# Optimization experiments

Measured on AMD Instinct MI355X. Metric: run time of the kernel, lower is better.

Reference implementation:

```python
import jax, jax.numpy as jnp
import numpy as np

N_NODES = 100000
N_EDGES = 200000
N_GRAPHS = 4000
F_IN = 44
H = 256
E = 512
L = 4


def setup_inputs() -> dict:
    key = jax.random.key(0)
    ks = jax.random.split(key, 16)
    x = jax.random.normal(ks[0], (N_NODES, F_IN), dtype=jnp.float32)
    edge_index = jax.random.randint(ks[1], (2, N_EDGES), 0, N_NODES)
    batch = jnp.sort(jax.random.randint(ks[2], (N_NODES,), 0, N_GRAPHS))
    s = lambda fan_in: 1.0 / np.sqrt(fan_in)
    W_atom = jax.random.uniform(ks[3], (F_IN, H), jnp.float32, -s(F_IN), s(F_IN))
    b_atom = jnp.zeros((H,), jnp.float32)
    W1 = jax.random.uniform(ks[4], (L, H, 2 * H), jnp.float32, -s(H), s(H))
    b1 = jnp.zeros((L, 2 * H), jnp.float32)
    W2 = jax.random.uniform(ks[5], (L, 2 * H, H), jnp.float32, -s(2 * H), s(2 * H))
    b2 = jnp.zeros((L, H), jnp.float32)
    Wf1 = jax.random.uniform(ks[6], (H, H), jnp.float32, -s(H), s(H))
    bf1 = jnp.zeros((H,), jnp.float32)
    Wf2 = jax.random.uniform(ks[7], (H, E), jnp.float32, -s(H), s(H))
    bf2 = jnp.zeros((E,), jnp.float32)
    return {"x": x, "edge_index": edge_index, "batch": batch,
            "W_atom": W_atom, "b_atom": b_atom,
            "W1": W1, "b1": b1, "W2": W2, "b2": b2,
            "Wf1": Wf1, "bf1": bf1, "Wf2": Wf2, "bf2": bf2}


def reference(x, edge_index, batch, W_atom, b_atom, W1, b1, W2, b2, Wf1, bf1, Wf2, bf2):
    src, dst = edge_index[0], edge_index[1]
    h = jax.nn.relu(x @ W_atom + b_atom)  # [N, H]
    for l in range(L):
        # GIN aggregation: agg_i = sum_{j->i} h_j ; eps=0 so node term is h_i itself
        agg = jax.ops.segment_sum(h[src], dst, num_segments=N_NODES)
        z = h + agg
        z = jax.nn.relu(z @ W1[l] + b1[l])
        z = z @ W2[l] + b2[l]
        h = jax.nn.relu(z)
    # global mean pool by graph id
    sums = jax.ops.segment_sum(h, batch, num_segments=N_GRAPHS)
    counts = jax.ops.segment_sum(jnp.ones((N_NODES,), h.dtype), batch, num_segments=N_GRAPHS)
    h_graph = sums / jnp.maximum(counts, 1.0)[:, None]  # [G, H]
    out = jax.nn.relu(h_graph @ Wf1 + bf1) @ Wf2 + bf2  # [G, E]
    return out
```

## Files before the change

### kernel.cpp

```cpp
#include <hip/hip_runtime.h>

#define N_NODES 100000
#define N_EDGES 200000
#define N_GRAPHS 4000
#define F_IN 44
#define HDIM 256
#define EDIM 512
#define NLAYERS 4

typedef float floatx4 __attribute__((ext_vector_type(4)));
typedef short bhalf8 __attribute__((ext_vector_type(8)));

__device__ __forceinline__ unsigned short f2bf(float f) {
    unsigned int u = __float_as_uint(f);
    u += 0x7FFFu + ((u >> 16) & 1u);
    return (unsigned short)(u >> 16);
}
__device__ __forceinline__ float bf2f(unsigned short s) {
    return __uint_as_float(((unsigned int)s) << 16);
}

__device__ __forceinline__ void gload16(const void* gsrc, void* ldst) {
    __builtin_amdgcn_global_load_lds(
        (const __attribute__((address_space(1))) void*)gsrc,
        (__attribute__((address_space(3))) void*)ldst, 16, 0, 0);
}

__global__ void zero_kernel(float* __restrict__ p, size_t n4) {
    size_t i = (size_t)blockIdx.x * blockDim.x + threadIdx.x;
    const size_t stride = (size_t)gridDim.x * blockDim.x;
    const float4 z = make_float4(0.f, 0.f, 0.f, 0.f);
    for (; i < n4; i += stride) ((float4*)p)[i] = z;
}

__global__ void xprep_kernel(const float* __restrict__ x, unsigned short* __restrict__ xb) {
    int idx = blockIdx.x * 256 + threadIdx.x;
    const int total = N_NODES * 16;
    const int stride = gridDim.x * 256;
    for (; idx < total; idx += stride) {
        const int n = idx >> 4, k4 = idx & 15;
        ushort4 v = make_ushort4(0, 0, 0, 0);
        if (k4 < F_IN / 4) {
            const float4 xv = *(const float4*)(x + (size_t)n * F_IN + k4 * 4);
            v.x = f2bf(xv.x); v.y = f2bf(xv.y); v.z = f2bf(xv.z); v.w = f2bf(xv.w);
        }
        *(ushort4*)(xb + (size_t)n * 64 + k4 * 4) = v;
    }
}

__global__ void hist_kernel(const int* __restrict__ dst, int* __restrict__ deg) {
    const int e = blockIdx.x * 256 + threadIdx.x;
    if (e < N_EDGES) atomicAdd(&deg[dst[e]], 1);
}

__global__ void scan1_kernel(const int* __restrict__ deg, int* __restrict__ row_ptr,
                             int* __restrict__ blk) {
    __shared__ int s[256];
    const int i = blockIdx.x * 256 + threadIdx.x;
    s[threadIdx.x] = (i < N_NODES) ? deg[i] : 0;
    __syncthreads();
    for (int off = 1; off < 256; off <<= 1) {
        int t = (threadIdx.x >= off) ? s[threadIdx.x - off] : 0;
        __syncthreads();
        s[threadIdx.x] += t;
        __syncthreads();
    }
    if (i < N_NODES) row_ptr[i + 1] = s[threadIdx.x];
    if (threadIdx.x == 255) blk[blockIdx.x] = s[255];
}

__global__ void scan2_kernel(int* __restrict__ blk, int nb) {
    if (threadIdx.x == 0 && blockIdx.x == 0) {
        int run = 0;
        for (int b = 0; b < nb; ++b) { const int t = blk[b]; blk[b] = run; run += t; }
    }
}

__global__ void scan3_kernel(int* __restrict__ row_ptr, const int* __restrict__ blk) {
    const int i = blockIdx.x * 256 + threadIdx.x;
    if (i < N_NODES) row_ptr[i + 1] += blk[i >> 8];
    if (i == 0) row_ptr[0] = 0;
}

__global__ void cursor_kernel(const int* __restrict__ row_ptr, int* __restrict__ cursor) {
    const int i = blockIdx.x * 256 + threadIdx.x;
    if (i < N_NODES) cursor[i] = row_ptr[i];
}

__global__ void fill_kernel(const int* __restrict__ src, const int* __restrict__ dst,
                            int* __restrict__ cursor, int* __restrict__ eids) {
    const int e = blockIdx.x * 256 + threadIdx.x;
    if (e < N_EDGES) {
        const int pos = atomicAdd(&cursor[dst[e]], 1);
        eids[pos] = src[e];
    }
}

__global__ void sort_kernel(const int* __restrict__ row_ptr, int* __restrict__ eids) {
    const int n = blockIdx.x * 256 + threadIdx.x;
    if (n < N_NODES) {
        const int s = row_ptr[n], e = row_ptr[n + 1];
        for (int i = s + 1; i < e; ++i) {
            const int v = eids[i];
            int j = i - 1;
            while (j >= s && eids[j] > v) { eids[j + 1] = eids[j]; --j; }
            eids[j + 1] = v;
        }
    }
}

__global__ void gather_kernel(const unsigned short* __restrict__ h,
                              const int* __restrict__ row_ptr,
                              const int* __restrict__ eids, unsigned short* __restrict__ z) {
    const int tid = threadIdx.x;
    const int n = blockIdx.x * 8 + (tid >> 5);
    const int t = tid & 31;
    const uint4* h4 = (const uint4*)h;
    const uint4 hv = h4[(size_t)n * 32 + t];
    float acc[8];
    acc[0] = bf2f((unsigned short)hv.x); acc[1] = bf2f((unsigned short)(hv.x >> 16));
    acc[2] = bf2f((unsigned short)hv.y); acc[3] = bf2f((unsigned short)(hv.y >> 16));
    acc[4] = bf2f((unsigned short)hv.z); acc[5] = bf2f((unsigned short)(hv.z >> 16));
    acc[6] = bf2f((unsigned short)hv.w); acc[7] = bf2f((unsigned short)(hv.w >> 16));
    const int s = row_ptr[n], e = row_ptr[n + 1];
    for (int i = s; i < e; ++i) {
        const uint4 v = h4[(size_t)eids[i] * 32 + t];
        acc[0] += bf2f((unsigned short)v.x); acc[1] += bf2f((unsigned short)(v.x >> 16));
        acc[2] += bf2f((unsigned short)v.y); acc[3] += bf2f((unsigned short)(v.y >> 16));
        acc[4] += bf2f((unsigned short)v.z); acc[5] += bf2f((unsigned short)(v.z >> 16));
        acc[6] += bf2f((unsigned short)v.w); acc[7] += bf2f((unsigned short)(v.w >> 16));
    }
    uint4 pk;
    pk.x = (unsigned int)f2bf(acc[0]) | ((unsigned int)f2bf(acc[1]) << 16);
    pk.y = (unsigned int)f2bf(acc[2]) | ((unsigned int)f2bf(acc[3]) << 16);
    pk.z = (unsigned int)f2bf(acc[4]) | ((unsigned int)f2bf(acc[5]) << 16);
    pk.w = (unsigned int)f2bf(acc[6]) | ((unsigned int)f2bf(acc[7]) << 16);
    ((uint4*)z)[(size_t)n * 32 + t] = pk;
}

__global__ void wprep_all(const float* __restrict__ W1, const float* __restrict__ W2,
                          const float* __restrict__ Wf1, const float* __restrict__ Wf2,
                          const float* __restrict__ Wa,
                          unsigned short* __restrict__ t1, unsigned short* __restrict__ t2,
                          unsigned short* __restrict__ tf1, unsigned short* __restrict__ tf2,
                          unsigned short* __restrict__ tat) {
    const int WSZ = HDIM * 2 * HDIM;
    const int T0 = 8 * WSZ;
    const int T1 = T0 + HDIM * HDIM;
    const int T2 = T1 + HDIM * EDIM;
    const int T3 = T2 + 64 * HDIM;
    const int stride = gridDim.x * 256;
    for (int idx = blockIdx.x * 256 + threadIdx.x; idx < T3; idx += stride) {
        if (idx < 4 * WSZ) {
            const int l = idx >> 17, e = idx & (WSZ - 1);
            const int k = e >> 9, n = e & 511;
            t1[(size_t)l * WSZ + n * HDIM + k] = f2bf(W1[idx]);
        } else if (idx < T0) {
            const int r = idx - 4 * WSZ;
            const int l = r >> 17, e = r & (WSZ - 1);
            const int k = e >> 8, n = e & 255;
            t2[(size_t)l * WSZ + n * EDIM + k] = f2bf(W2[r]);
        } else if (idx < T1) {
            const int e = idx - T0;
            const int k = e >> 8, n = e & 255;
            tf1[n * HDIM + k] = f2bf(Wf1[e]);
        } else if (idx < T2) {
            const int e = idx - T1;
            const int k = e >> 9, n = e & 511;
            tf2[n * HDIM + k] = f2bf(Wf2[e]);
        } else {
            const int e = idx - T2;
            const int n = e >> 6, k = e & 63;
            tat[n * 64 + k] = (k < F_IN) ? f2bf(Wa[k * HDIM + n]) : (unsigned short)0;
        }
    }
}

__global__ __launch_bounds__(256, 2)
void fused_layer(const unsigned short* __restrict__ zin, const unsigned short* __restrict__ T1,
                 const unsigned short* __restrict__ T2, const float* __restrict__ b1,
                 const float* __restrict__ b2, unsigned short* __restrict__ H, int M) {
    __shared__ __align__(16) unsigned short lds[37888];
    unsigned short* sA  = lds;
    unsigned short* sB1 = lds + 8192;
    unsigned short* zb  = lds + 12288;
    unsigned short* sB2 = lds + 21504;

    const int G = gridDim.x;
    int wg = blockIdx.x;
    {
        const int q = G >> 3, r = G & 7;
        const int xx = wg & 7, o = wg >> 3;
        wg = (xx < r ? xx * (q + 1) : r * (q + 1) + (xx - r) * q) + o;
    }
    const int row0 = wg << 7;

    const int tid = threadIdx.x;
    const int lane = tid & 63;
    const int w = tid >> 6;
    const int wr = w >> 1, wc = w & 1;
    const int lr = lane & 15;
    const int l4 = lane >> 4;
    const int rgrp = l4 * 4;
    const int srow = tid >> 3;
    const int sgran = ((tid & 7) ^ (srow & 7)) << 3;

    floatx4 acc_h[4][8];
#pragma unroll
    for (int m = 0; m < 4; ++m)
#pragma unroll
        for (int n = 0; n < 8; ++n) acc_h[m][n] = (floatx4){0.f, 0.f, 0.f, 0.f};

#pragma unroll 1
    for (int c = 0; c < 8; ++c) {
        floatx4 acc_z[4][2];
#pragma unroll
        for (int m = 0; m < 4; ++m)
#pragma unroll
            for (int n = 0; n < 2; ++n) acc_z[m][n] = (floatx4){0.f, 0.f, 0.f, 0.f};

#pragma unroll 1
        for (int t = 0; t < 4; ++t) {
            __syncthreads();
#pragma unroll
            for (int p = 0; p < 4; ++p) {
                const int r = (p << 5) + srow;
                int ar = row0 + r; if (ar >= M) ar = M - 1;
                gload16(zin + (size_t)ar * 256 + (t << 6) + sgran, &sA[(p << 11) + (w << 9)]);
            }
#pragma unroll
            for (int p = 0; p < 2; ++p) {
                const int r = (p << 5) + srow;
                gload16(T1 + (size_t)((c << 6) + r) * 256 + (t << 6) + sgran,
                        &sB1[(p << 11) + (w << 9)]);
            }
            if (t == 0) {
#pragma unroll
                for (int p = 0; p < 8; ++p) {
                    const int r = (p << 5) + srow;
                    gload16(T2 + (size_t)r * 512 + (c << 6) + sgran,
                            &sB2[(p << 11) + (w << 9)]);
                }
            }
            __syncthreads();
#pragma unroll
            for (int s = 0; s < 2; ++s) {
                const int pg = (((s << 2) + l4) ^ (lr & 7)) << 3;
                bhalf8 fa[4], fb[2];
#pragma unroll
                for (int m = 0; m < 4; ++m)
                    fa[m] = *(const bhalf8*)&sA[((wr << 6) + (m << 4) + lr) * 64 + pg];
#pragma unroll
                for (int n = 0; n < 2; ++n)
                    fb[n] = *(const bhalf8*)&sB1[((wc << 5) + (n << 4) + lr) * 64 + pg];
#pragma unroll
                for (int m = 0; m < 4; ++m)
#pragma unroll
                    for (int n = 0; n < 2; ++n)
                        acc_z[m][n] = __builtin_amdgcn_mfma_f32_16x16x32_bf16(fa[m], fb[n], acc_z[m][n], 0, 0, 0);
            }
        }

#pragma unroll
        for (int n = 0; n < 2; ++n) {
            const int ck = (wc << 5) + (n << 4) + lr;
            const float bv = b1[(c << 6) + ck];
#pragma unroll
            for (int m = 0; m < 4; ++m) {
                const int rw = (wr << 6) + (m << 4) + rgrp;
#pragma unroll
                for (int j = 0; j < 4; ++j)
                    zb[(rw + j) * 72 + ck] = f2bf(fmaxf(acc_z[m][n][j] + bv, 0.f));
            }
        }
        __syncthreads();

#pragma unroll
        for (int s = 0; s < 2; ++s) {
            const int pg = (((s << 2) + l4) ^ (lr & 7)) << 3;
            const int zg = ((s << 2) + l4) << 3;
            bhalf8 fa[4], fb[8];
#pragma unroll
            for (int m = 0; m < 4; ++m)
                fa[m] = *(const bhalf8*)&zb[((wr << 6) + (m << 4) + lr) * 72 + zg];
#pragma unroll
            for (int n = 0; n < 8; ++n)
                fb[n] = *(const bhalf8*)&sB2[((wc << 7) + (n << 4) + lr) * 64 + pg];
#pragma unroll
            for (int m = 0; m < 4; ++m)
#pragma unroll
                for (int n = 0; n < 8; ++n)
                    acc_h[m][n] = __builtin_amdgcn_mfma_f32_16x16x32_bf16(fa[m], fb[n], acc_h[m][n], 0, 0, 0);
        }
    }

    __syncthreads();
#pragma unroll
    for (int n = 0; n < 8; ++n) {
        const int colt = (wc << 7) + (n << 4) + lr;
        const float bv = b2[colt];
#pragma unroll
        for (int m = 0; m < 4; ++m) {
            const int rwt = (wr << 6) + (m << 4) + rgrp;
#pragma unroll
            for (int j = 0; j < 4; ++j)
                lds[(rwt + j) * 264 + colt] = f2bf(fmaxf(acc_h[m][n][j] + bv, 0.f));
        }
    }
    __syncthreads();
    const int orow = tid >> 1;
    const int ohalf = (tid & 1) << 7;
    if (row0 + orow < M) {
        const uint4* sp = (const uint4*)(lds + orow * 264 + ohalf);
        uint4* dp = (uint4*)(H + (size_t)(row0 + orow) * 256 + ohalf);
#pragma unroll
        for (int q = 0; q < 16; ++q) dp[q] = sp[q];
    }
}

template <int OUT>
__global__ __launch_bounds__(256)
void gemm_mfma(const unsigned short* __restrict__ A, const unsigned short* __restrict__ BT,
               const float* __restrict__ bias, float* __restrict__ C,
               unsigned short* __restrict__ Z, int M, int N, int KK) {
    __shared__ __align__(16) unsigned short lds_all[32768];

    const int ncol = N >> 7;
    const int G = gridDim.x;
    int wg = blockIdx.x;
    {
        const int q = G >> 3, r = G & 7;
        const int xx = wg & 7, o = wg >> 3;
        wg = (xx < r ? xx * (q + 1) : r * (q + 1) + (xx - r) * q) + o;
    }
    const int col0 = (wg % ncol) << 7;
    const int row0 = (wg / ncol) << 7;

    const int tid = threadIdx.x;
    const int lane = tid & 63;
    const int w = tid >> 6;
    const int wr = w >> 1, wc = w & 1;
    const int lr = lane & 15;
    const int l4 = lane >> 4;
    const int srow = tid >> 3;
    const int sgran = ((tid & 7) ^ (srow & 7)) << 3;

    floatx4 acc[4][4];
#pragma unroll
    for (int m = 0; m < 4; ++m)
#pragma unroll
        for (int n = 0; n < 4; ++n) acc[m][n] = (floatx4){0.f, 0.f, 0.f, 0.f};

    const int NT = KK >> 6;

    auto stage = [&](int t, int b) {
        const int k0 = t << 6;
        unsigned short* la = &lds_all[b * 16384];
        unsigned short* lb = la + 8192;
#pragma unroll
        for (int pass = 0; pass < 4; ++pass) {
            const int r = (pass << 5) + srow;
            int ar = row0 + r; if (ar >= M) ar = M - 1;
            gload16(A + (size_t)ar * KK + k0 + sgran, &la[(pass << 11) + (w << 9)]);
            gload16(BT + (size_t)(col0 + r) * KK + k0 + sgran, &lb[(pass << 11) + (w << 9)]);
        }
    };

    stage(0, 0);
    if (NT > 1) stage(1, 1);
    for (int t = 0; t < NT; ++t) {
        const int cur = t & 1;
        if (t + 1 < NT) {
            asm volatile("s_waitcnt vmcnt(8)" ::: "memory");
        } else {
            asm volatile("s_waitcnt vmcnt(0)" ::: "memory");
        }
        __builtin_amdgcn_s_barrier();

        const unsigned short* la = &lds_all[cur * 16384];
        const unsigned short* lb = la + 8192;
#pragma unroll
        for (int s = 0; s < 2; ++s) {
            const int pg = (((s << 2) + l4) ^ (lr & 7)) << 3;
            bhalf8 fa[4], fb[4];
#pragma unroll
            for (int m = 0; m < 4; ++m)
                fa[m] = *(const bhalf8*)&la[((wr << 6) + (m << 4) + lr) * 64 + pg];
#pragma unroll
            for (int n = 0; n < 4; ++n)
                fb[n] = *(const bhalf8*)&lb[((wc << 6) + (n << 4) + lr) * 64 + pg];
#pragma unroll
            for (int m = 0; m < 4; ++m)
#pragma unroll
                for (int n = 0; n < 4; ++n)
                    acc[m][n] = __builtin_amdgcn_mfma_f32_16x16x32_bf16(fa[m], fb[n], acc[m][n], 0, 0, 0);
        }

        __builtin_amdgcn_s_barrier();
        if (t + 2 < NT) stage(t + 2, cur);
    }

    const int rgrp = l4 * 4;
    if (OUT == 2) {
        __syncthreads();
#pragma unroll
        for (int n = 0; n < 4; ++n) {
            const int colt = (wc << 6) + (n << 4) + lr;
            const float bv = bias[col0 + colt];
#pragma unroll
            for (int m = 0; m < 4; ++m) {
                const int rwt = (wr << 6) + (m << 4) + rgrp;
#pragma unroll
                for (int j = 0; j < 4; ++j)
                    lds_all[(rwt + j) * 136 + colt] = f2bf(fmaxf(acc[m][n][j] + bv, 0.f));
            }
        }
        __syncthreads();
        const int orow = tid >> 1;
        const int ocol = (tid & 1) << 6;
        if (row0 + orow < M) {
            const uint4* sp = (const uint4*)(lds_all + orow * 136 + ocol);
            uint4* dp = (uint4*)(Z + (size_t)(row0 + orow) * N + col0 + ocol);
#pragma unroll
            for (int q = 0; q < 8; ++q) dp[q] = sp[q];
        }
    } else {
#pragma unroll
        for (int n = 0; n < 4; ++n) {
            const int col = col0 + (wc << 6) + (n << 4) + lr;
            const float bv = bias[col];
#pragma unroll
            for (int m = 0; m < 4; ++m) {
                const int rw = row0 + (wr << 6) + (m << 4) + rgrp;
#pragma unroll
                for (int j = 0; j < 4; ++j) {
                    const int row = rw + j;
                    if (row < M) C[(size_t)row * N + col] = acc[m][n][j] + bv;
                }
            }
        }
    }
}

__global__ void pool_kernel(const unsigned short* __restrict__ h,
                            const int* __restrict__ batch,
                            unsigned short* __restrict__ gz) {
    __shared__ int sse[2];
    const int g = blockIdx.x;
    if (threadIdx.x < 2) {
        const int target = g + threadIdx.x;
        int lo = 0, hi = N_NODES;
        while (lo < hi) {
            const int mid = (lo + hi) >> 1;
            if (batch[mid] < target) lo = mid + 1; else hi = mid;
        }
        sse[threadIdx.x] = lo;
    }
    __syncthreads();
    const int s = sse[0], e = sse[1];
    const int j = threadIdx.x;
    float acc = 0.f;
    for (int n = s; n < e; ++n) acc += bf2f(h[(size_t)n * HDIM + j]);
    const float v = acc * ((e > s) ? 1.f / (float)(e - s) : 1.f);
    gz[(size_t)g * HDIM + j] = f2bf(v);
}

extern "C" void kernel_launch(void* const* d_in, const int* in_sizes, int n_in,
                              void* d_out, int out_size, void* d_ws, size_t ws_size,
                              hipStream_t stream) {
    const float* x      = (const float*)d_in[0];
    const int*   eidx   = (const int*)d_in[1];
    const int*   batch  = (const int*)d_in[2];
    const float* W_atom = (const float*)d_in[3];
    const float* b_atom = (const float*)d_in[4];
    const float* W1     = (const float*)d_in[5];
    const float* b1     = (const float*)d_in[6];
    const float* W2     = (const float*)d_in[7];
    const float* b2     = (const float*)d_in[8];
    const float* Wf1    = (const float*)d_in[9];
    const float* bf1    = (const float*)d_in[10];
    const float* Wf2    = (const float*)d_in[11];
    const float* bf2    = (const float*)d_in[12];
    float* out = (float*)d_out;

    const int* src = eidx;
    const int* dst = eidx + N_EDGES;

    const size_t NH = (size_t)N_NODES * HDIM;
    const int WSZ = HDIM * 2 * HDIM;

    char* base = (char*)d_ws;
    size_t off = 0;
    unsigned short* h = (unsigned short*)(base + off);      off += NH * 2;
    unsigned short* zin = (unsigned short*)(base + off);    off += NH * 2;
    unsigned short* xb = (unsigned short*)(base + off);     off += (size_t)N_NODES * 64 * 2;
    int* deg     = (int*)(base + off);            off += (size_t)N_NODES * 4;
    int* row_ptr = (int*)(base + off);            off += (size_t)(N_NODES + 1) * 4;
    int* cursor  = (int*)(base + off);            off += (size_t)N_NODES * 4;
    int* eids    = (int*)(base + off);            off += (size_t)N_EDGES * 4;
    int* blk     = (int*)(base + off);            off += 512 * 4;
    off = (off + 255) & ~(size_t)255;
    unsigned short* t1 = (unsigned short*)(base + off); off += (size_t)NLAYERS * WSZ * 2;
    unsigned short* t2 = (unsigned short*)(base + off); off += (size_t)NLAYERS * WSZ * 2;
    unsigned short* tf1 = (unsigned short*)(base + off); off += (size_t)HDIM * HDIM * 2;
    unsigned short* tf2 = (unsigned short*)(base + off); off += (size_t)HDIM * EDIM * 2;
    unsigned short* tat = (unsigned short*)(base + off); off += (size_t)HDIM * 64 * 2;
    off = (off + 255) & ~(size_t)255;

    const size_t GH = (size_t)N_GRAPHS * HDIM;
    unsigned short* hg  = zin;
    unsigned short* hg1 = zin + GH;

    const int nb = (N_NODES + 255) / 256;
    const int nrow128 = (N_NODES + 127) / 128;

    xprep_kernel<<<1024, 256, 0, stream>>>(x, xb);
    wprep_all<<<1024, 256, 0, stream>>>(W1, W2, Wf1, Wf2, W_atom, t1, t2, tf1, tf2, tat);

    zero_kernel<<<128, 256, 0, stream>>>((float*)deg, N_NODES / 4);
    hist_kernel<<<(N_EDGES + 255) / 256, 256, 0, stream>>>(dst, deg);
    scan1_kernel<<<nb, 256, 0, stream>>>(deg, row_ptr, blk);
    scan2_kernel<<<1, 64, 0, stream>>>(blk, nb);
    scan3_kernel<<<nb, 256, 0, stream>>>(row_ptr, blk);
    cursor_kernel<<<nb, 256, 0, stream>>>(row_ptr, cursor);
    fill_kernel<<<(N_EDGES + 255) / 256, 256, 0, stream>>>(src, dst, cursor, eids);
    sort_kernel<<<nb, 256, 0, stream>>>(row_ptr, eids);

    gemm_mfma<2><<<2 * nrow128, 256, 0, stream>>>(
        xb, tat, b_atom, nullptr, h, N_NODES, HDIM, 64);

    for (int l = 0; l < NLAYERS; ++l) {
        gather_kernel<<<N_NODES / 8, 256, 0, stream>>>(h, row_ptr, eids, zin);
        fused_layer<<<nrow128, 256, 0, stream>>>(
            zin, t1 + (size_t)l * WSZ, t2 + (size_t)l * WSZ,
            b1 + (size_t)l * 2 * HDIM, b2 + (size_t)l * HDIM, h, N_NODES);
    }

    pool_kernel<<<N_GRAPHS, HDIM, 0, stream>>>(h, batch, hg);

    gemm_mfma<2><<<2 * ((N_GRAPHS + 127) / 128), 256, 0, stream>>>(
        hg, tf1, bf1, nullptr, hg1, N_GRAPHS, HDIM, HDIM);
    gemm_mfma<0><<<4 * ((N_GRAPHS + 127) / 128), 256, 0, stream>>>(
        hg1, tf2, bf2, out, nullptr, N_GRAPHS, EDIM, HDIM);
}
```

Measured before the change: 702.9 us.

## Use 512-thread blocks with 8 waves in fused GIN layer kernel

Doubles the fused MLP layer's workgroup from 4 to 8 waves. Each wave now owns a 64x16 slice of the first GEMM and a 64x64 slice of the second, which halves the per-wave accumulator registers and spreads the LDS staging loads across more threads. The aim is more waves in flight per CU to hide latency. In exchange, each wave reuses its fragments less (fewer MFMAs per LDS read), and barrier cost grows with the larger block.

```diff
diff --git a/kernel.cpp b/kernel.cpp
--- a/kernel.cpp
+++ b/kernel.cpp
@@ -176,7 +176,7 @@
     }
 }
 
-__global__ __launch_bounds__(256, 2)
+__global__ __launch_bounds__(512)
 void fused_layer(const unsigned short* __restrict__ zin, const unsigned short* __restrict__ T1,
                  const unsigned short* __restrict__ T2, const float* __restrict__ b1,
                  const float* __restrict__ b2, unsigned short* __restrict__ H, int M) {
@@ -198,79 +198,71 @@
     const int tid = threadIdx.x;
     const int lane = tid & 63;
     const int w = tid >> 6;
-    const int wr = w >> 1, wc = w & 1;
+    const int wr = w >> 2, wc = w & 3;
     const int lr = lane & 15;
     const int l4 = lane >> 4;
     const int rgrp = l4 * 4;
     const int srow = tid >> 3;
     const int sgran = ((tid & 7) ^ (srow & 7)) << 3;
 
-    floatx4 acc_h[4][8];
+    floatx4 acc_h[4][4];
 #pragma unroll
     for (int m = 0; m < 4; ++m)
 #pragma unroll
-        for (int n = 0; n < 8; ++n) acc_h[m][n] = (floatx4){0.f, 0.f, 0.f, 0.f};
+        for (int n = 0; n < 4; ++n) acc_h[m][n] = (floatx4){0.f, 0.f, 0.f, 0.f};
 
 #pragma unroll 1
     for (int c = 0; c < 8; ++c) {
-        floatx4 acc_z[4][2];
-#pragma unroll
-        for (int m = 0; m < 4; ++m)
-#pragma unroll
-            for (int n = 0; n < 2; ++n) acc_z[m][n] = (floatx4){0.f, 0.f, 0.f, 0.f};
+        floatx4 acc_z[4];
+#pragma unroll
+        for (int m = 0; m < 4; ++m) acc_z[m] = (floatx4){0.f, 0.f, 0.f, 0.f};
 
 #pragma unroll 1
         for (int t = 0; t < 4; ++t) {
             __syncthreads();
 #pragma unroll
-            for (int p = 0; p < 4; ++p) {
-                const int r = (p << 5) + srow;
+            for (int p = 0; p < 2; ++p) {
+                const int r = (p << 6) + srow;
                 int ar = row0 + r; if (ar >= M) ar = M - 1;
-                gload16(zin + (size_t)ar * 256 + (t << 6) + sgran, &sA[(p << 11) + (w << 9)]);
-            }
-#pragma unroll
-            for (int p = 0; p < 2; ++p) {
-                const int r = (p << 5) + srow;
-                gload16(T1 + (size_t)((c << 6) + r) * 256 + (t << 6) + sgran,
-                        &sB1[(p << 11) + (w << 9)]);
+                gload16(zin + (size_t)ar * 256 + (t << 6) + sgran,
+                        &sA[(p << 12) + (w << 9)]);
+            }
+            {
+                gload16(T1 + (size_t)((c << 6) + srow) * 256 + (t << 6) + sgran,
+                        &sB1[(w << 9)]);
             }
             if (t == 0) {
 #pragma unroll
-                for (int p = 0; p < 8; ++p) {
-                    const int r = (p << 5) + srow;
+                for (int p = 0; p < 4; ++p) {
+                    const int r = (p << 6) + srow;
                     gload16(T2 + (size_t)r * 512 + (c << 6) + sgran,
-                            &sB2[(p << 11) + (w << 9)]);
+                            &sB2[(p << 12) + (w << 9)]);
                 }
             }
             __syncthreads();
 #pragma unroll
             for (int s = 0; s < 2; ++s) {
                 const int pg = (((s << 2) + l4) ^ (lr & 7)) << 3;
-                bhalf8 fa[4], fb[2];
+                bhalf8 fa[4], fb;
 #pragma unroll
                 for (int m = 0; m < 4; ++m)
                     fa[m] = *(const bhalf8*)&sA[((wr << 6) + (m << 4) + lr) * 64 + pg];
-#pragma unroll
-                for (int n = 0; n < 2; ++n)
-                    fb[n] = *(const bhalf8*)&sB1[((wc << 5) + (n << 4) + lr) * 64 + pg];
+                fb = *(const bhalf8*)&sB1[((wc << 4) + lr) * 64 + pg];
 #pragma unroll
                 for (int m = 0; m < 4; ++m)
-#pragma unroll
-                    for (int n = 0; n < 2; ++n)
-                        acc_z[m][n] = __builtin_amdgcn_mfma_f32_16x16x32_bf16(fa[m], fb[n], acc_z[m][n], 0, 0, 0);
-            }
-        }
-
-#pragma unroll
-        for (int n = 0; n < 2; ++n) {
-            const int ck = (wc << 5) + (n << 4) + lr;
+                    acc_z[m] = __builtin_amdgcn_mfma_f32_16x16x32_bf16(fa[m], fb, acc_z[m], 0, 0, 0);
+            }
+        }
+
+        {
+            const int ck = (wc << 4) + lr;
             const float bv = b1[(c << 6) + ck];
 #pragma unroll
             for (int m = 0; m < 4; ++m) {
                 const int rw = (wr << 6) + (m << 4) + rgrp;
 #pragma unroll
                 for (int j = 0; j < 4; ++j)
-                    zb[(rw + j) * 72 + ck] = f2bf(fmaxf(acc_z[m][n][j] + bv, 0.f));
+                    zb[(rw + j) * 72 + ck] = f2bf(fmaxf(acc_z[m][j] + bv, 0.f));
             }
         }
         __syncthreads();
@@ -279,25 +271,25 @@
         for (int s = 0; s < 2; ++s) {
             const int pg = (((s << 2) + l4) ^ (lr & 7)) << 3;
             const int zg = ((s << 2) + l4) << 3;
-            bhalf8 fa[4], fb[8];
+            bhalf8 fa[4], fb[4];
 #pragma unroll
             for (int m = 0; m < 4; ++m)
                 fa[m] = *(const bhalf8*)&zb[((wr << 6) + (m << 4) + lr) * 72 + zg];
 #pragma unroll
-            for (int n = 0; n < 8; ++n)
-                fb[n] = *(const bhalf8*)&sB2[((wc << 7) + (n << 4) + lr) * 64 + pg];
+            for (int n = 0; n < 4; ++n)
+                fb[n] = *(const bhalf8*)&sB2[((wc << 6) + (n << 4) + lr) * 64 + pg];
 #pragma unroll
             for (int m = 0; m < 4; ++m)
 #pragma unroll
-                for (int n = 0; n < 8; ++n)
+                for (int n = 0; n < 4; ++n)
                     acc_h[m][n] = __builtin_amdgcn_mfma_f32_16x16x32_bf16(fa[m], fb[n], acc_h[m][n], 0, 0, 0);
         }
     }
 
     __syncthreads();
 #pragma unroll
-    for (int n = 0; n < 8; ++n) {
-        const int colt = (wc << 7) + (n << 4) + lr;
+    for (int n = 0; n < 4; ++n) {
+        const int colt = (wc << 6) + (n << 4) + lr;
         const float bv = b2[colt];
 #pragma unroll
         for (int m = 0; m < 4; ++m) {
@@ -308,13 +300,13 @@
         }
     }
     __syncthreads();
-    const int orow = tid >> 1;
-    const int ohalf = (tid & 1) << 7;
+    const int orow = tid >> 2;
+    const int oq = (tid & 3) << 6;
     if (row0 + orow < M) {
-        const uint4* sp = (const uint4*)(lds + orow * 264 + ohalf);
-        uint4* dp = (uint4*)(H + (size_t)(row0 + orow) * 256 + ohalf);
-#pragma unroll
-        for (int q = 0; q < 16; ++q) dp[q] = sp[q];
+        const uint4* sp = (const uint4*)(lds + orow * 264 + oq);
+        uint4* dp = (uint4*)(H + (size_t)(row0 + orow) * 256 + oq);
+#pragma unroll
+        for (int q = 0; q < 8; ++q) dp[q] = sp[q];
     }
 }
 
@@ -531,7 +523,7 @@
 
     for (int l = 0; l < NLAYERS; ++l) {
         gather_kernel<<<N_NODES / 8, 256, 0, stream>>>(h, row_ptr, eids, zin);
-        fused_layer<<<nrow128, 256, 0, stream>>>(
+        fused_layer<<<nrow128, 512, 0, stream>>>(
             zin, t1 + (size_t)l * WSZ, t2 + (size_t)l * WSZ,
             b1 + (size_t)l * 2 * HDIM, b2 + (size_t)l * HDIM, h, N_NODES);
     }
```

Measured after the change: 936.1 us. +33.2%, slower.
